# Optimization experiments

Hardware: AMD Instinct MI355X
Metric: run time of the kernel (lower is better)

The kernel has to match this reference:

```python
import jax, jax.numpy as jnp
import numpy as np
from jax import lax

FIELD = 32          # backbone receptive-field stride (field_size of ResNet50)
K = 3               # number of anchor sizes
ANCHOR_PX = (32, 64, 96)
POOL = 2
TILES = 3
NMS_IOU = 0.3
R_POST = 512        # post-NMS proposal cap (static shape for jit)
IMG = 1536
MG = IMG // FIELD   # 48x48 feature map
C = 256
HID = 1024


def setup_inputs() -> dict:
    key = jax.random.key(0)
    ks = jax.random.split(key, 6)
    # create_anchors: per feature cell (grid step FIELD) and per anchor size,
    # row = [x_upper_left, y_upper_left, width, height]
    grid = np.arange(MG, dtype=np.float32) * FIELD + FIELD / 2.0  # cell centers
    cy, cx, aa = np.meshgrid(grid, grid, np.array(ANCHOR_PX, np.float32), indexing='ij')
    anchors = np.stack([cx - aa / 2, cy - aa / 2, aa, aa], axis=-1).reshape(-1, 4).astype(np.float32)
    return {
        'features': jax.random.normal(ks[0], (1, MG, MG, C), jnp.float32),
        'anchors': jnp.asarray(anchors),
        'W_obj': jax.random.normal(ks[1], (C, 2 * K), jnp.float32) * 0.1,
        'b_obj': jnp.zeros((2 * K,), jnp.float32),
        'W_reg': jax.random.normal(ks[2], (C, 4 * K), jnp.float32) * 0.01,
        'b_reg': jnp.zeros((4 * K,), jnp.float32),
        'W_fc1': jax.random.normal(ks[3], (TILES * TILES * C, HID), jnp.float32) * 0.02,
        'b_fc1': jnp.zeros((HID,), jnp.float32),
        'W_fc2': jax.random.normal(ks[4], (HID, 4), jnp.float32) * 0.01,
        'b_fc2': jnp.zeros((4,), jnp.float32),
    }


def _map_outputs(out, anchors):
    # out: [M, N, K*D] RPN output; returns [A, D], one row per anchor
    apx = jnp.asarray(ANCHOR_PX, jnp.int32)
    k = jnp.argmax(anchors[:, 3].astype(jnp.int32)[:, None] == apx[None, :], axis=1)
    px = ((anchors[:, 0] + anchors[:, 2] * 0.5) / FIELD).astype(jnp.int32)
    py = ((anchors[:, 1] + anchors[:, 3] * 0.5) / FIELD).astype(jnp.int32)
    M, N, _ = out.shape
    r = out.reshape(M, N, K, -1)
    return r[py, px, k]


def _unparameterize(reg, anchors):
    cxa = anchors[:, 0] + anchors[:, 2] * 0.5
    cya = anchors[:, 1] + anchors[:, 3] * 0.5
    cx = reg[:, 0] * anchors[:, 2] + cxa
    cy = reg[:, 1] * anchors[:, 3] + cya
    w = anchors[:, 2] * jnp.exp(reg[:, 2])
    h = anchors[:, 3] * jnp.exp(reg[:, 3])
    return jnp.stack([cx - w * 0.5, cy - h * 0.5, w, h], axis=1)


def _clip_boxes(b, W, H):
    x1 = jnp.clip(b[:, 0], 0.0, W)
    y1 = jnp.clip(b[:, 1], 0.0, H)
    x2 = jnp.clip(b[:, 0] + b[:, 2], 0.0, W)
    y2 = jnp.clip(b[:, 1] + b[:, 3], 0.0, H)
    return jnp.stack([x1, y1, x2 - x1, y2 - y1], axis=1)


def _pairwise_iou(b):
    x1, y1 = b[:, 0], b[:, 1]
    x2, y2 = b[:, 0] + b[:, 2], b[:, 1] + b[:, 3]
    iw = jnp.maximum(0.0, jnp.minimum(x2[:, None], x2[None, :]) - jnp.maximum(x1[:, None], x1[None, :]))
    ih = jnp.maximum(0.0, jnp.minimum(y2[:, None], y2[None, :]) - jnp.maximum(y1[:, None], y1[None, :]))
    inter = iw * ih
    area = (x2 - x1) * (y2 - y1)
    return inter / (area[:, None] + area[None, :] - inter + 1e-8)


def _roialign(fmap, boxes):
    # fmap: [M, N, C]; boxes: [R, 4] xywh -> [R, TILES, TILES, C]
    M, N, Cc = fmap.shape
    S = TILES * POOL
    offs = (jnp.arange(S, dtype=boxes.dtype) + 0.5) / S
    fx = jnp.clip((boxes[:, 0:1] + offs[None, :] * boxes[:, 2:3]) / FIELD - 0.5, 0.0, N - 1.0)
    fy = jnp.clip((boxes[:, 1:2] + offs[None, :] * boxes[:, 3:4]) / FIELD - 0.5, 0.0, M - 1.0)
    x0 = jnp.floor(fx).astype(jnp.int32); x1 = jnp.minimum(x0 + 1, N - 1); wx = fx - x0
    y0 = jnp.floor(fy).astype(jnp.int32); y1 = jnp.minimum(y0 + 1, M - 1); wy = fy - y0
    def g(yi, xi):
        return fmap[yi[:, :, None], xi[:, None, :]]  # [R, S, S, C]
    wX = wx[:, None, :, None]; wY = wy[:, :, None, None]
    v = (g(y0, x0) * (1 - wY) * (1 - wX) + g(y0, x1) * (1 - wY) * wX
         + g(y1, x0) * wY * (1 - wX) + g(y1, x1) * wY * wX)
    R = boxes.shape[0]
    return v.reshape(R, TILES, POOL, TILES, POOL, Cc).mean(axis=(2, 4))


def reference(features, anchors, W_obj, b_obj, W_reg, b_reg, W_fc1, b_fc1, W_fc2, b_fc2):
    fmap = features[0]  # [M, N, C]
    out_obj = fmap @ W_obj + b_obj   # [M, N, 2K]
    out_reg = fmap @ W_reg + b_reg   # [M, N, 4K]
    rpn_obj = jax.nn.softmax(_map_outputs(out_obj, anchors), axis=1)  # [A, 2]
    rpn_reg = _map_outputs(out_reg, anchors)                          # [A, 4]
    boxes = _clip_boxes(_unparameterize(rpn_reg, anchors), float(IMG), float(IMG))
    scores = rpn_obj[:, 1]
    A = boxes.shape[0]
    # NMS (sequential greedy suppression on score-sorted boxes)
    order = jnp.argsort(-scores)
    iou_mat = lax.stop_gradient(_pairwise_iou(boxes[order]))  # [A, A], index selection is non-diff
    idx = jnp.arange(A)
    def body(i, keep):
        sup = jnp.any((iou_mat[i] > NMS_IOU) & keep & (idx < i))
        return keep.at[i].set(~sup)
    keep = lax.fori_loop(0, A, body, jnp.zeros((A,), bool))
    masked = jnp.where(keep, scores[order], -1e9)
    _, topi = lax.top_k(masked, R_POST)
    sel = order[topi]
    sel_boxes = boxes[sel]
    sel_obj = rpn_obj[sel]
    pooled = _roialign(fmap, sel_boxes)            # [R, TILES, TILES, C]
    flat = pooled.reshape(R_POST, -1)
    h = jax.nn.relu(flat @ W_fc1 + b_fc1)
    align_reg = h @ W_fc2 + b_fc2                  # [R, 4]
    align_boxes = _unparameterize(align_reg, sel_boxes)
    # concat (rpn_obj, rpn_boxes, align_boxes) -> [R, 10]
    return jnp.concatenate([sel_obj, sel_boxes, align_boxes], axis=1)
```

## Files before the change

kernel.cpp:

```cpp
#include <hip/hip_runtime.h>
#include <hip/hip_bf16.h>

typedef unsigned long long ull;

#define MGRID 48
#define CCH   256
#define NCELL 2304
#define NA    6912
#define NW    108
#define NHID  1024
#define KFC   2304
#define RPOST 512
#define IMGF  1536.0f

typedef __attribute__((ext_vector_type(8))) short short8v;
typedef __attribute__((ext_vector_type(4))) float f32x4;

__global__ __launch_bounds__(256) void rpn_wcvt(const float* __restrict__ feat,
    const float* __restrict__ Wobj, const float* __restrict__ bobj,
    const float* __restrict__ Wreg, const float* __restrict__ breg,
    float* __restrict__ rpn, const float* __restrict__ Wfc1,
    ushort* __restrict__ Wt){
  if (blockIdx.x >= 162){
    __shared__ float tile[32][33];
    int bid = blockIdx.x - 162;
    int bx = bid & 31;
    int by = bid >> 5;
    int tx = threadIdx.x & 31, ty = threadIdx.x >> 5;
    #pragma unroll
    for (int it=0; it<4; ++it)
      tile[ty + 8*it][tx] = Wfc1[(size_t)(by*32 + ty + 8*it)*NHID + bx*32 + tx];
    __syncthreads();
    #pragma unroll
    for (int it=0; it<4; ++it){
      __hip_bfloat16 b = __float2bfloat16(tile[tx][ty + 8*it]);
      Wt[(size_t)(bx*32 + ty + 8*it)*KFC + by*32 + tx] = *(ushort*)&b;
    }
    return;
  }
  int g = blockIdx.x*256 + threadIdx.x;
  int cell = g / 18, o = g % 18;
  const float* W; int stride; float acc;
  if (o < 6){ W = Wobj + o; stride = 6;  acc = bobj[o];   }
  else      { W = Wreg + (o-6); stride = 12; acc = breg[o-6]; }
  const float4* x4 = (const float4*)(feat + cell*CCH);
  #pragma unroll 4
  for (int c4=0;c4<CCH/4;++c4){
    float4 xv = x4[c4];
    acc += xv.x*W[(4*c4+0)*stride];
    acc += xv.y*W[(4*c4+1)*stride];
    acc += xv.z*W[(4*c4+2)*stride];
    acc += xv.w*W[(4*c4+3)*stride];
  }
  rpn[cell*18 + o] = acc;
}

__global__ __launch_bounds__(256) void anchor_prep(const float* __restrict__ rpn,
    const float* __restrict__ anchors, float* __restrict__ probs,
    float* __restrict__ boxes, ull* __restrict__ keys){
  int a = blockIdx.x*256 + threadIdx.x;
  int cell = a/3, k = a%3;
  const float* rc = rpn + cell*18;
  float l0 = rc[2*k], l1 = rc[2*k+1];
  float m  = fmaxf(l0,l1);
  float e0 = expf(l0-m), e1 = expf(l1-m);
  float s  = e0 + e1;
  float p0 = e0/s, p1 = e1/s;
  probs[a*2+0] = p0; probs[a*2+1] = p1;
  float4 an = ((const float4*)anchors)[a];
  float r0 = rc[6+4*k+0], r1 = rc[6+4*k+1], r2 = rc[6+4*k+2], r3 = rc[6+4*k+3];
  float cxa = an.x + an.z*0.5f, cya = an.y + an.w*0.5f;
  float cx = r0*an.z + cxa, cy = r1*an.w + cya;
  float w  = an.z*expf(r2),  hh = an.w*expf(r3);
  float bx = cx - w*0.5f, by = cy - hh*0.5f;
  float x1 = fminf(fmaxf(bx,      0.0f), IMGF);
  float y1 = fminf(fmaxf(by,      0.0f), IMGF);
  float x2 = fminf(fmaxf(bx + w,  0.0f), IMGF);
  float y2 = fminf(fmaxf(by + hh, 0.0f), IMGF);
  float4 bo; bo.x = x1; bo.y = y1; bo.z = x2 - x1; bo.w = y2 - y1;
  ((float4*)boxes)[a] = bo;
  keys[a] = ((ull)__float_as_uint(p1) << 32) | (unsigned)(NA-1-a);
}

__global__ __launch_bounds__(256) void rank_part(const ull* __restrict__ keys,
                                                 int* __restrict__ part){
  __shared__ ull lk[256];
  int t = threadIdx.x;
  int ib = blockIdx.x, jb = blockIdx.y;
  lk[t] = keys[jb*256 + t];
  int i = ib*256 + t;
  ull ki = keys[i];
  __syncthreads();
  int cnt = 0;
  #pragma unroll 16
  for (int j=0;j<256;++j) cnt += (lk[j] > ki) ? 1 : 0;
  part[jb*NA + i] = cnt;
}

__global__ __launch_bounds__(256) void rank_scatter(const int* __restrict__ part,
    const float* __restrict__ boxes, int* __restrict__ ord, float* __restrict__ sboxes){
  int i = blockIdx.x*256 + threadIdx.x;
  int r = 0;
  #pragma unroll
  for (int jb=0;jb<27;++jb) r += part[jb*NA + i];
  ord[r] = i;
  ((float4*)sboxes)[r] = ((const float4*)boxes)[i];
}

#define NQ 5993
__global__ __launch_bounds__(256) void iou_mask(const float* __restrict__ sboxes,
                                                ull* __restrict__ maskT){
  int g = blockIdx.x*256 + threadIdx.x;
  int q = g >> 6;
  if (q >= NQ) return;
  int w = (int)((sqrtf(8.0f*(float)q + 9.0f) - 3.0f) * 0.5f);
  if (w > 107) w = 107;
  while (w < 107 && (w+1)*(w+4)/2 <= q) ++w;
  while (w > 0 && w*(w+3)/2 > q) --w;
  int ib = q - w*(w+3)/2;
  int i = ib*64 + (g & 63);
  float4 bi = ((const float4*)sboxes)[i];
  float x1i = bi.x, y1i = bi.y;
  float x2i = bi.x + bi.z, y2i = bi.y + bi.w;
  float ai  = (x2i - x1i) * (y2i - y1i);
  const float4* bj4 = (const float4*)sboxes + w*64;
  ull bits = 0;
  #pragma unroll 8
  for (int jj=0;jj<64;++jj){
    float4 bj = bj4[jj];
    float x1j = bj.x, y1j = bj.y;
    float x2j = bj.x + bj.z, y2j = bj.y + bj.w;
    float aj  = (x2j - x1j) * (y2j - y1j);
    float iw = fmaxf(fminf(x2i,x2j) - fmaxf(x1i,x1j), 0.0f);
    float ih = fmaxf(fminf(y2i,y2j) - fmaxf(y1i,y1j), 0.0f);
    float inter = iw*ih;
    float den = ai + aj - inter + 1e-8f;
    if (inter > 0.3f*den) bits |= (1ull<<jj);
  }
  maskT[(size_t)w*NA + i] = bits;
}

__global__ __launch_bounds__(256) void nms(const ull* __restrict__ maskT,
    const int* __restrict__ ord, const float* __restrict__ sboxes,
    const float* __restrict__ probs, float* __restrict__ out,
    float* __restrict__ selb){
  __shared__ ull remv[NW];
  __shared__ ull keepw[NW];
  __shared__ ull kb_sh[2];
  __shared__ int selpos[RPOST];
  __shared__ int base_sh[NW];
  __shared__ int cnt_sh, done_sh;
  int t = threadIdx.x;
  if (t < NW){ remv[t] = 0ull; keepw[t] = 0ull; }
  if (t == 0){ cnt_sh = 0; done_sh = 0; kb_sh[0] = 0ull; kb_sh[1] = 0ull; }
  __syncthreads();

  ull dg_cur = 0, srow_cur = 0, kb_prev = 0;
  if (t < 64) dg_cur = maskT[t];

  for (int c = 0; c < NW; ++c){
    if (t < 64){
      ull dg_nxt = 0, srow_nxt = 0;
      if (c+1 < NW){
        dg_nxt   = maskT[(size_t)(c+1)*NA + (size_t)(c+1)*64 + t];
        srow_nxt = maskT[(size_t)c*NA + (size_t)(c+1)*64 + t];
      }
      ull w0 = remv[c];
      bool dec  = ((w0 >> t) & 1ull) || ((srow_cur & kb_prev) != 0ull);
      bool kept = false;
      ull sup = dg_cur & ((1ull << t) - 1ull);
      for (;;){
        ull K = __ballot(kept);
        ull D = __ballot(dec);
        if (D == ~0ull) break;
        if (!dec){
          if (sup & K)                 { dec = true; }
          else if ((sup & ~D) == 0ull) { dec = true; kept = true; }
        }
      }
      ull kb = __ballot(kept);
      int cnt0 = cnt_sh;
      ull below = kb & ((1ull << t) - 1ull);
      int myrank = cnt0 + __popcll(below);
      if (kept && myrank < RPOST) selpos[myrank] = c*64 + t;
      if (t == 0){
        kb_sh[c & 1] = kb;
        keepw[c] = kb;
        int nc = cnt0 + __popcll(kb);
        if (nc >= RPOST){ nc = RPOST; done_sh = 1; }
        cnt_sh = nc;
      }
      kb_prev = kb; dg_cur = dg_nxt; srow_cur = srow_nxt;
    } else {
      int u = t - 64;
      int wp = c + 1 + u;
      if (c >= 1 && wp < NW){
        ull kbp = kb_sh[(c-1) & 1];
        if (kbp){
          const ull* row = maskT + (size_t)wp*NA + (size_t)(c-1)*64;
          ull acc = remv[wp];
          #pragma unroll
          for (int b=0;b<64;++b)
            acc |= (0ull - ((kbp >> b) & 1ull)) & row[b];
          remv[wp] = acc;
        }
      }
    }
    __syncthreads();
    if (done_sh) break;
  }
  __syncthreads();
  int cnt0 = cnt_sh;
  if (cnt0 < RPOST){
    if (t < NW){
      int s = 0;
      for (int w2=0; w2<t; ++w2) s += __popcll(~keepw[w2]);
      base_sh[t] = s;
    }
    __syncthreads();
    for (int p = t; p < NA; p += 256){
      int w2 = p >> 6, b = p & 63;
      ull kw = keepw[w2];
      if (!((kw >> b) & 1ull)){
        int rank = cnt0 + base_sh[w2] + __popcll(~kw & ((1ull << b) - 1ull));
        if (rank < RPOST) selpos[rank] = p;
      }
    }
  }
  __syncthreads();
  for (int s=t; s<RPOST; s+=256){
    int pos = selpos[s];
    int orig = ord[pos];
    float4 b = ((const float4*)sboxes)[pos];
    out[s*10+0] = probs[orig*2+0];
    out[s*10+1] = probs[orig*2+1];
    out[s*10+2] = b.x; out[s*10+3] = b.y; out[s*10+4] = b.z; out[s*10+5] = b.w;
    ((float4*)selb)[s] = b;
  }
}

__global__ __launch_bounds__(256) void roialign(const float* __restrict__ feat,
    const float* __restrict__ selb, __hip_bfloat16* __restrict__ pooled){
  int r = blockIdx.x, c = threadIdx.x;
  float4 b = ((const float4*)selb)[r];
  int x0[6], x1[6], y0[6], y1[6];
  float wx[6], wy[6];
  #pragma unroll
  for (int s=0;s<6;++s){
    float off = ((float)s + 0.5f) / 6.0f;
    float fx = (b.x + off*b.z) / 32.0f - 0.5f;
    fx = fminf(fmaxf(fx, 0.0f), 47.0f);
    int xx0 = (int)floorf(fx);
    x0[s] = xx0; x1[s] = min(xx0+1, 47); wx[s] = fx - (float)xx0;
    float fy = (b.y + off*b.w) / 32.0f - 0.5f;
    fy = fminf(fmaxf(fy, 0.0f), 47.0f);
    int yy0 = (int)floorf(fy);
    y0[s] = yy0; y1[s] = min(yy0+1, 47); wy[s] = fy - (float)yy0;
  }
  #pragma unroll
  for (int ty=0;ty<3;++ty){
    #pragma unroll
    for (int tx=0;tx<3;++tx){
      float sum = 0.0f;
      #pragma unroll
      for (int py=0;py<2;++py){
        #pragma unroll
        for (int px=0;px<2;++px){
          int sy = ty*2+py, sx = tx*2+px;
          float wxx = wx[sx], wyy = wy[sy];
          float v00 = feat[(y0[sy]*MGRID + x0[sx])*CCH + c];
          float v01 = feat[(y0[sy]*MGRID + x1[sx])*CCH + c];
          float v10 = feat[(y1[sy]*MGRID + x0[sx])*CCH + c];
          float v11 = feat[(y1[sy]*MGRID + x1[sx])*CCH + c];
          sum += v00*(1.0f-wyy)*(1.0f-wxx) + v01*(1.0f-wyy)*wxx
               + v10*wyy*(1.0f-wxx)        + v11*wyy*wxx;
        }
      }
      pooled[((r*9) + ty*3 + tx)*CCH + c] = __float2bfloat16(sum * 0.25f);
    }
  }
}

__global__ __launch_bounds__(256) void fc1_mfma(const ushort* __restrict__ A,
    const ushort* __restrict__ Bt, const float* __restrict__ bias,
    float* __restrict__ Hp){
  __shared__ ushort As[4096];
  __shared__ ushort Bs[4096];
  const int t = threadIdx.x;
  const int bn = blockIdx.x, bm = blockIdx.y, bz = blockIdx.z;
  const int wv = t >> 6, lane = t & 63;
  const int wm = (wv >> 1) * 32, wn = (wv & 1) * 32;

  const int r0 = t >> 3, kc = t & 7;
  const int r1 = r0 + 32;
  const int kbase = bz * 144;
  const float4* gA0 = (const float4*)A  + (size_t)(bm*64 + r0)*288 + kbase + kc;
  const float4* gA1 = (const float4*)A  + (size_t)(bm*64 + r1)*288 + kbase + kc;
  const float4* gB0 = (const float4*)Bt + (size_t)(bn*64 + r0)*288 + kbase + kc;
  const float4* gB1 = (const float4*)Bt + (size_t)(bn*64 + r1)*288 + kbase + kc;
  float4* sA0 = (float4*)As + ((r0<<3) | (kc ^ (r0&7)));
  float4* sA1 = (float4*)As + ((r1<<3) | (kc ^ (r1&7)));
  float4* sB0 = (float4*)Bs + ((r0<<3) | (kc ^ (r0&7)));
  float4* sB1 = (float4*)Bs + ((r1<<3) | (kc ^ (r1&7)));

  const int fr = lane & 15, fkg = lane >> 4;
  const int arow0 = wm + fr,      arow1 = wm + 16 + fr;
  const int brow0 = wn + fr,      brow1 = wn + 16 + fr;

  f32x4 acc00{}, acc01{}, acc10{}, acc11{};

  const int KT = 18;
  float4 pa0 = gA0[0], pa1 = gA1[0], pb0 = gB0[0], pb1 = gB1[0];
  for (int kt = 0; kt < KT; ++kt){
    __syncthreads();
    *sA0 = pa0; *sA1 = pa1; *sB0 = pb0; *sB1 = pb1;
    if (kt + 1 < KT){
      pa0 = gA0[(kt+1)*8]; pa1 = gA1[(kt+1)*8];
      pb0 = gB0[(kt+1)*8]; pb1 = gB1[(kt+1)*8];
    }
    __syncthreads();
    #pragma unroll
    for (int kk2 = 0; kk2 < 2; ++kk2){
      int kidx = fkg + kk2*4;
      short8v a0 = *(const short8v*)(As + ((((arow0<<3) | (kidx ^ (arow0&7)))) << 3));
      short8v a1 = *(const short8v*)(As + ((((arow1<<3) | (kidx ^ (arow1&7)))) << 3));
      short8v b0 = *(const short8v*)(Bs + ((((brow0<<3) | (kidx ^ (brow0&7)))) << 3));
      short8v b1 = *(const short8v*)(Bs + ((((brow1<<3) | (kidx ^ (brow1&7)))) << 3));
      acc00 = __builtin_amdgcn_mfma_f32_16x16x32_bf16(a0, b0, acc00, 0, 0, 0);
      acc01 = __builtin_amdgcn_mfma_f32_16x16x32_bf16(a0, b1, acc01, 0, 0, 0);
      acc10 = __builtin_amdgcn_mfma_f32_16x16x32_bf16(a1, b0, acc10, 0, 0, 0);
      acc11 = __builtin_amdgcn_mfma_f32_16x16x32_bf16(a1, b1, acc11, 0, 0, 0);
    }
  }
  float* H = Hp + (size_t)bz * 512 * NHID;
  const int orow = bm*64 + wm + (lane>>4)*4;
  const int ocol = bn*64 + wn + (lane&15);
  #pragma unroll
  for (int i=0;i<2;++i){
    #pragma unroll
    for (int j=0;j<2;++j){
      f32x4 a = (i==0) ? ((j==0)?acc00:acc01) : ((j==0)?acc10:acc11);
      #pragma unroll
      for (int reg=0;reg<4;++reg){
        int row = orow + i*16 + reg;
        int col = ocol + j*16;
        float v = a[reg] + (bz == 0 ? bias[col] : 0.0f);
        H[(size_t)row*NHID + col] = v;
      }
    }
  }
}

__global__ __launch_bounds__(64) void fc2(const float* __restrict__ h0,
    const float* __restrict__ h1, const float* __restrict__ W2,
    const float* __restrict__ b2, const float* __restrict__ selb,
    float* __restrict__ out){
  int r = blockIdx.x, lane = threadIdx.x;
  float a0=0,a1=0,a2=0,a3=0;
  #pragma unroll 4
  for (int it=0; it<16; ++it){
    int k = it*64 + lane;
    float hv = fmaxf(h0[(size_t)r*NHID + k] + h1[(size_t)r*NHID + k], 0.0f);
    float4 w = ((const float4*)W2)[k];
    a0 += hv*w.x; a1 += hv*w.y; a2 += hv*w.z; a3 += hv*w.w;
  }
  #pragma unroll
  for (int off=32; off>0; off>>=1){
    a0 += __shfl_down(a0, off);
    a1 += __shfl_down(a1, off);
    a2 += __shfl_down(a2, off);
    a3 += __shfl_down(a3, off);
  }
  if (lane == 0){
    float4 b = ((const float4*)selb)[r];
    float r0 = a0 + b2[0], r1 = a1 + b2[1], r2 = a2 + b2[2], r3 = a3 + b2[3];
    float cxa = b.x + b.z*0.5f, cya = b.y + b.w*0.5f;
    float cx = r0*b.z + cxa, cy = r1*b.w + cya;
    float w  = b.z*expf(r2),  hh = b.w*expf(r3);
    out[r*10+6] = cx - w*0.5f;
    out[r*10+7] = cy - hh*0.5f;
    out[r*10+8] = w;
    out[r*10+9] = hh;
  }
}

extern "C" void kernel_launch(void* const* d_in, const int* in_sizes, int n_in,
                              void* d_out, int out_size, void* d_ws, size_t ws_size,
                              hipStream_t stream) {
  const float* feat    = (const float*)d_in[0];
  const float* anchors = (const float*)d_in[1];
  const float* Wobj    = (const float*)d_in[2];
  const float* bobj    = (const float*)d_in[3];
  const float* Wreg    = (const float*)d_in[4];
  const float* breg    = (const float*)d_in[5];
  const float* Wfc1    = (const float*)d_in[6];
  const float* bfc1    = (const float*)d_in[7];
  const float* Wfc2    = (const float*)d_in[8];
  const float* bfc2    = (const float*)d_in[9];
  float* out = (float*)d_out;
  char* ws = (char*)d_ws;

  float* rpn    = (float*)(ws + 0);
  float* probs  = (float*)(ws + 165888);
  float* boxes  = (float*)(ws + 221184);
  ull*   keys   = (ull*)  (ws + 331776);
  int*   ord    = (int*)  (ws + 387072);
  float* sboxes = (float*)(ws + 414720);
  int*   part   = (int*)  (ws + 525312);
  ull*   maskT  = (ull*)  (ws + 1271808);
  float* selb   = (float*)(ws + 7243776);
  __hip_bfloat16* pooled = (__hip_bfloat16*)(ws + 7251968);
  float* h      = (float*)(ws + 9611264);
  ushort* Wt    = (ushort*)(ws + 13805568);

  float* h0 = h;
  float* h1 = h + 512*NHID;

  hipLaunchKernelGGL(rpn_wcvt,     dim3(2466),    dim3(256), 0, stream, feat, Wobj, bobj, Wreg, breg, rpn, Wfc1, Wt);
  hipLaunchKernelGGL(anchor_prep,  dim3(27),      dim3(256), 0, stream, rpn, anchors, probs, boxes, keys);
  hipLaunchKernelGGL(rank_part,    dim3(27,27),   dim3(256), 0, stream, keys, part);
  hipLaunchKernelGGL(rank_scatter, dim3(27),      dim3(256), 0, stream, part, boxes, ord, sboxes);
  hipLaunchKernelGGL(iou_mask,     dim3(1499),    dim3(256), 0, stream, sboxes, maskT);
  hipLaunchKernelGGL(nms,          dim3(1),       dim3(256), 0, stream, maskT, ord, sboxes, probs, out, selb);
  hipLaunchKernelGGL(roialign,     dim3(512),     dim3(256), 0, stream, feat, selb, pooled);
  hipLaunchKernelGGL(fc1_mfma,     dim3(16,8,2),  dim3(256), 0, stream, (const ushort*)pooled, Wt, bfc1, h);
  hipLaunchKernelGGL(fc2,          dim3(512),     dim3(64),  0, stream, h0, h1, Wfc2, bfc2, selb, out);
}
```

Baseline: 91.21 us.

## Fuse anchor prep into RPN head and prefetch NMS suppression rows

Merges the anchor decode/softmax/key kernel into the RPN head kernel, keeping the RPN outputs in shared memory instead of a global buffer and removing one launch. In the single-block NMS, the helper threads now split each pending suppression word across two threads and load the mask rows for the next iteration into registers one step ahead. They then OR their partial results into the shared word with atomics. This targets the serial latency of global loads inside the NMS chunk loop, at the cost of a larger block of 320 threads, more registers and shared atomics.

Result: faster. 88.76 us (-2.7%).

```diff
diff --git a/kernel.cpp b/kernel.cpp
--- a/kernel.cpp
+++ b/kernel.cpp
@@ -12,21 +12,24 @@
 #define KFC   2304
 #define RPOST 512
 #define IMGF  1536.0f
+#define NQ    5993
 
 typedef __attribute__((ext_vector_type(8))) short short8v;
 typedef __attribute__((ext_vector_type(4))) float f32x4;
 
-__global__ __launch_bounds__(256) void rpn_wcvt(const float* __restrict__ feat,
+__global__ __launch_bounds__(256) void rpn_anchor_wcvt(const float* __restrict__ feat,
     const float* __restrict__ Wobj, const float* __restrict__ bobj,
     const float* __restrict__ Wreg, const float* __restrict__ breg,
-    float* __restrict__ rpn, const float* __restrict__ Wfc1,
-    ushort* __restrict__ Wt){
-  if (blockIdx.x >= 162){
+    const float* __restrict__ anchors, float* __restrict__ probs,
+    float* __restrict__ boxes, ull* __restrict__ keys,
+    const float* __restrict__ Wfc1, ushort* __restrict__ Wt){
+  int t = threadIdx.x;
+  if (blockIdx.x >= 192){
     __shared__ float tile[32][33];
-    int bid = blockIdx.x - 162;
+    int bid = blockIdx.x - 192;
     int bx = bid & 31;
     int by = bid >> 5;
-    int tx = threadIdx.x & 31, ty = threadIdx.x >> 5;
+    int tx = t & 31, ty = t >> 5;
     #pragma unroll
     for (int it=0; it<4; ++it)
       tile[ty + 8*it][tx] = Wfc1[(size_t)(by*32 + ty + 8*it)*NHID + bx*32 + tx];
@@ -38,48 +41,49 @@
     }
     return;
   }
-  int g = blockIdx.x*256 + threadIdx.x;
-  int cell = g / 18, o = g % 18;
-  const float* W; int stride; float acc;
-  if (o < 6){ W = Wobj + o; stride = 6;  acc = bobj[o];   }
-  else      { W = Wreg + (o-6); stride = 12; acc = breg[o-6]; }
-  const float4* x4 = (const float4*)(feat + cell*CCH);
-  #pragma unroll 4
-  for (int c4=0;c4<CCH/4;++c4){
-    float4 xv = x4[c4];
-    acc += xv.x*W[(4*c4+0)*stride];
-    acc += xv.y*W[(4*c4+1)*stride];
-    acc += xv.z*W[(4*c4+2)*stride];
-    acc += xv.w*W[(4*c4+3)*stride];
-  }
-  rpn[cell*18 + o] = acc;
-}
-
-__global__ __launch_bounds__(256) void anchor_prep(const float* __restrict__ rpn,
-    const float* __restrict__ anchors, float* __restrict__ probs,
-    float* __restrict__ boxes, ull* __restrict__ keys){
-  int a = blockIdx.x*256 + threadIdx.x;
-  int cell = a/3, k = a%3;
-  const float* rc = rpn + cell*18;
-  float l0 = rc[2*k], l1 = rc[2*k+1];
-  float m  = fmaxf(l0,l1);
-  float e0 = expf(l0-m), e1 = expf(l1-m);
-  float s  = e0 + e1;
-  float p0 = e0/s, p1 = e1/s;
-  probs[a*2+0] = p0; probs[a*2+1] = p1;
-  float4 an = ((const float4*)anchors)[a];
-  float r0 = rc[6+4*k+0], r1 = rc[6+4*k+1], r2 = rc[6+4*k+2], r3 = rc[6+4*k+3];
-  float cxa = an.x + an.z*0.5f, cya = an.y + an.w*0.5f;
-  float cx = r0*an.z + cxa, cy = r1*an.w + cya;
-  float w  = an.z*expf(r2),  hh = an.w*expf(r3);
-  float bx = cx - w*0.5f, by = cy - hh*0.5f;
-  float x1 = fminf(fmaxf(bx,      0.0f), IMGF);
-  float y1 = fminf(fmaxf(by,      0.0f), IMGF);
-  float x2 = fminf(fmaxf(bx + w,  0.0f), IMGF);
-  float y2 = fminf(fmaxf(by + hh, 0.0f), IMGF);
-  float4 bo; bo.x = x1; bo.y = y1; bo.z = x2 - x1; bo.w = y2 - y1;
-  ((float4*)boxes)[a] = bo;
-  keys[a] = ((ull)__float_as_uint(p1) << 32) | (unsigned)(NA-1-a);
+  __shared__ float rpn_lds[12*18];
+  int cell0 = blockIdx.x * 12;
+  if (t < 216){
+    int lc = t / 18, o = t % 18;
+    const float* W; int stride; float acc;
+    if (o < 6){ W = Wobj + o; stride = 6;  acc = bobj[o];   }
+    else      { W = Wreg + (o-6); stride = 12; acc = breg[o-6]; }
+    const float4* x4 = (const float4*)(feat + (cell0 + lc)*CCH);
+    #pragma unroll 4
+    for (int c4=0;c4<CCH/4;++c4){
+      float4 xv = x4[c4];
+      acc += xv.x*W[(4*c4+0)*stride];
+      acc += xv.y*W[(4*c4+1)*stride];
+      acc += xv.z*W[(4*c4+2)*stride];
+      acc += xv.w*W[(4*c4+3)*stride];
+    }
+    rpn_lds[t] = acc;
+  }
+  __syncthreads();
+  if (t < 36){
+    int a = cell0*3 + t;
+    int k = t % 3;
+    const float* rc = rpn_lds + (t/3)*18;
+    float l0 = rc[2*k], l1 = rc[2*k+1];
+    float m  = fmaxf(l0,l1);
+    float e0 = expf(l0-m), e1 = expf(l1-m);
+    float s  = e0 + e1;
+    float p0 = e0/s, p1 = e1/s;
+    probs[a*2+0] = p0; probs[a*2+1] = p1;
+    float4 an = ((const float4*)anchors)[a];
+    float r0 = rc[6+4*k+0], r1 = rc[6+4*k+1], r2 = rc[6+4*k+2], r3 = rc[6+4*k+3];
+    float cxa = an.x + an.z*0.5f, cya = an.y + an.w*0.5f;
+    float cx = r0*an.z + cxa, cy = r1*an.w + cya;
+    float w  = an.z*expf(r2),  hh = an.w*expf(r3);
+    float bx = cx - w*0.5f, by = cy - hh*0.5f;
+    float x1 = fminf(fmaxf(bx,      0.0f), IMGF);
+    float y1 = fminf(fmaxf(by,      0.0f), IMGF);
+    float x2 = fminf(fmaxf(bx + w,  0.0f), IMGF);
+    float y2 = fminf(fmaxf(by + hh, 0.0f), IMGF);
+    float4 bo; bo.x = x1; bo.y = y1; bo.z = x2 - x1; bo.w = y2 - y1;
+    ((float4*)boxes)[a] = bo;
+    keys[a] = ((ull)__float_as_uint(p1) << 32) | (unsigned)(NA-1-a);
+  }
 }
 
 __global__ __launch_bounds__(256) void rank_part(const ull* __restrict__ keys,
@@ -107,7 +111,6 @@
   ((float4*)sboxes)[r] = ((const float4*)boxes)[i];
 }
 
-#define NQ 5993
 __global__ __launch_bounds__(256) void iou_mask(const float* __restrict__ sboxes,
                                                 ull* __restrict__ maskT){
   int g = blockIdx.x*256 + threadIdx.x;
@@ -140,7 +143,7 @@
   maskT[(size_t)w*NA + i] = bits;
 }
 
-__global__ __launch_bounds__(256) void nms(const ull* __restrict__ maskT,
+__global__ __launch_bounds__(320) void nms(const ull* __restrict__ maskT,
     const int* __restrict__ ord, const float* __restrict__ sboxes,
     const float* __restrict__ probs, float* __restrict__ out,
     float* __restrict__ selb){
@@ -156,7 +159,14 @@
   __syncthreads();
 
   ull dg_cur = 0, srow_cur = 0, kb_prev = 0;
+  ulonglong2 pre[16];
+  #pragma unroll
+  for (int b=0;b<16;++b){ pre[b].x = 0ull; pre[b].y = 0ull; }
   if (t < 64) dg_cur = maskT[t];
+
+  const int u  = t - 64;
+  const int pw = u >> 1;
+  const int h  = u & 1;
 
   for (int c = 0; c < NW; ++c){
     if (t < 64){
@@ -192,18 +202,25 @@
       }
       kb_prev = kb; dg_cur = dg_nxt; srow_cur = srow_nxt;
     } else {
-      int u = t - 64;
-      int wp = c + 1 + u;
-      if (c >= 1 && wp < NW){
+      int wpc = c + 1 + pw;
+      if (c >= 1 && wpc < NW){
         ull kbp = kb_sh[(c-1) & 1];
         if (kbp){
-          const ull* row = maskT + (size_t)wp*NA + (size_t)(c-1)*64;
-          ull acc = remv[wp];
+          ull acc = 0;
           #pragma unroll
-          for (int b=0;b<64;++b)
-            acc |= (0ull - ((kbp >> b) & 1ull)) & row[b];
-          remv[wp] = acc;
+          for (int b=0;b<16;++b){
+            acc |= (0ull - ((kbp >> (h*32 + 2*b))   & 1ull)) & pre[b].x;
+            acc |= (0ull - ((kbp >> (h*32 + 2*b+1)) & 1ull)) & pre[b].y;
+          }
+          if (acc) atomicOr(&remv[wpc], acc);
         }
+      }
+      int wpn = c + 2 + pw;
+      if (c+1 < NW && wpn < NW){
+        const ulonglong2* src =
+          (const ulonglong2*)(maskT + (size_t)wpn*NA + (size_t)c*64) + h*16;
+        #pragma unroll
+        for (int b=0;b<16;++b) pre[b] = src[b];
       }
     }
     __syncthreads();
@@ -218,7 +235,7 @@
       base_sh[t] = s;
     }
     __syncthreads();
-    for (int p = t; p < NA; p += 256){
+    for (int p = t; p < NA; p += 320){
       int w2 = p >> 6, b = p & 63;
       ull kw = keepw[w2];
       if (!((kw >> b) & 1ull)){
@@ -228,7 +245,7 @@
     }
   }
   __syncthreads();
-  for (int s=t; s<RPOST; s+=256){
+  for (int s=t; s<RPOST; s+=320){
     int pos = selpos[s];
     int orig = ord[pos];
     float4 b = ((const float4*)sboxes)[pos];
@@ -400,7 +417,6 @@
   float* out = (float*)d_out;
   char* ws = (char*)d_ws;
 
-  float* rpn    = (float*)(ws + 0);
   float* probs  = (float*)(ws + 165888);
   float* boxes  = (float*)(ws + 221184);
   ull*   keys   = (ull*)  (ws + 331776);
@@ -416,12 +432,12 @@
   float* h0 = h;
   float* h1 = h + 512*NHID;
 
-  hipLaunchKernelGGL(rpn_wcvt,     dim3(2466),    dim3(256), 0, stream, feat, Wobj, bobj, Wreg, breg, rpn, Wfc1, Wt);
-  hipLaunchKernelGGL(anchor_prep,  dim3(27),      dim3(256), 0, stream, rpn, anchors, probs, boxes, keys);
+  hipLaunchKernelGGL(rpn_anchor_wcvt, dim3(2496),   dim3(256), 0, stream,
+                     feat, Wobj, bobj, Wreg, breg, anchors, probs, boxes, keys, Wfc1, Wt);
   hipLaunchKernelGGL(rank_part,    dim3(27,27),   dim3(256), 0, stream, keys, part);
   hipLaunchKernelGGL(rank_scatter, dim3(27),      dim3(256), 0, stream, part, boxes, ord, sboxes);
   hipLaunchKernelGGL(iou_mask,     dim3(1499),    dim3(256), 0, stream, sboxes, maskT);
-  hipLaunchKernelGGL(nms,          dim3(1),       dim3(256), 0, stream, maskT, ord, sboxes, probs, out, selb);
+  hipLaunchKernelGGL(nms,          dim3(1),       dim3(320), 0, stream, maskT, ord, sboxes, probs, out, selb);
   hipLaunchKernelGGL(roialign,     dim3(512),     dim3(256), 0, stream, feat, selb, pooled);
   hipLaunchKernelGGL(fc1_mfma,     dim3(16,8,2),  dim3(256), 0, stream, (const ushort*)pooled, Wt, bfc1, h);
   hipLaunchKernelGGL(fc2,          dim3(512),     dim3(64),  0, stream, h0, h1, Wfc2, bfc2, selb, out);
```
